# Performance work log

Measured on AMD Instinct MI355X. Metric: run time of the kernel, lower is better.

The kernel has to match this reference:

```python
import jax, jax.numpy as jnp
import numpy as np

N_NODES = 50000
N_EDGES = 1600000
IN_DIM = 128
HEADS = 8
OUT_C = 16  # per-head channels; HEADS*OUT_C == IN_DIM -> residual active
NEG_SLOPE = 0.2
BN_EPS = 1e-5


def setup_inputs() -> dict:
    key = jax.random.key(0)
    ks = jax.random.split(key, 8)
    x = jax.random.normal(ks[0], (N_NODES, IN_DIM), dtype=jnp.float32)
    edge_index = jax.random.randint(ks[1], (2, N_EDGES), 0, N_NODES, dtype=jnp.int64)
    # GATConv params (PyG: shared lin for src/dst on single-tensor input)
    W = jax.random.normal(ks[2], (IN_DIM, HEADS * OUT_C), dtype=jnp.float32) / np.sqrt(IN_DIM)
    att_src = jax.random.normal(ks[3], (HEADS, OUT_C), dtype=jnp.float32) / np.sqrt(OUT_C)
    att_dst = jax.random.normal(ks[4], (HEADS, OUT_C), dtype=jnp.float32) / np.sqrt(OUT_C)
    bias = jnp.zeros((HEADS * OUT_C,), dtype=jnp.float32)
    # BatchNorm1d affine params
    gamma = jnp.ones((HEADS * OUT_C,), dtype=jnp.float32)
    beta = jnp.zeros((HEADS * OUT_C,), dtype=jnp.float32)
    return {"x": x, "edge_index": edge_index, "W": W, "att_src": att_src,
            "att_dst": att_dst, "bias": bias, "gamma": gamma, "beta": beta}


def reference(x, edge_index, W, att_src, att_dst, bias, gamma, beta):
    N = x.shape[0]
    H, C = att_src.shape
    src, dst = edge_index[0], edge_index[1]

    xl = (x @ W).reshape(N, H, C)                      # [N,H,C]
    a_src = jnp.sum(xl * att_src[None], axis=-1)       # [N,H]
    a_dst = jnp.sum(xl * att_dst[None], axis=-1)       # [N,H]

    e = jax.nn.leaky_relu(a_src[src] + a_dst[dst], NEG_SLOPE)  # [E,H]
    # segment softmax over incoming edges of each dst node
    m = jax.ops.segment_max(e, dst, num_segments=N)    # [N,H], -inf for empty
    m = jnp.where(jnp.isfinite(m), m, 0.0)
    ex = jnp.exp(e - m[dst])                           # [E,H]
    denom = jax.ops.segment_sum(ex, dst, num_segments=N)
    alpha = ex / (denom[dst] + 1e-16)                  # [E,H]

    out = jax.ops.segment_sum(alpha[:, :, None] * xl[src], dst, num_segments=N)  # [N,H,C]
    h = out.reshape(N, H * C) + bias

    # BatchNorm1d (training mode: batch statistics, biased variance)
    mean = jnp.mean(h, axis=0)
    var = jnp.mean((h - mean) ** 2, axis=0)
    h = (h - mean) * jax.lax.rsqrt(var + BN_EPS) * gamma + beta

    h = jax.nn.relu(h)
    return x + h  # residual (in_dim == H*C)
```

## Files before the change

kernel.cpp:

```cpp
#include <hip/hip_runtime.h>
#include <hip/hip_fp16.h>
#include <math.h>

#define N_NODES 50000
#define N_EDGES 1600000
#define DIM 128
#define HEADS 8
#define NEG_SLOPE 0.2f
#define BN_EPS 1e-5f

typedef _Float16 f16x8 __attribute__((ext_vector_type(8)));
typedef float f32x4 __attribute__((ext_vector_type(4)));

__global__ void k_wprep(const float* __restrict__ W, __half* __restrict__ Wh,
                        int* __restrict__ bcur, float* __restrict__ gsums) {
    const int t = threadIdx.x;
    if (blockIdx.x == 0 && t < 256) bcur[t] = 0;
    if (blockIdx.x == 1 && t < 256) gsums[t] = 0.f;
    const int tid = blockIdx.x * 256 + t;
    const int g = tid >> 6;
    const int lane = tid & 63;
    const int nt = g >> 2, kt = g & 3;
    const int q = lane >> 4, n = lane & 15;
    #pragma unroll
    for (int j = 0; j < 8; ++j)
        Wh[(size_t)(g * 64 + lane) * 8 + j] =
            __float2half(W[(kt * 32 + q * 8 + j) * DIM + nt * 16 + n]);
}

__global__ __launch_bounds__(256) void k_lin(const float* __restrict__ x,
                      const __half* __restrict__ Wh, const float* __restrict__ att_s,
                      const float* __restrict__ att_d, __half* __restrict__ xlh,
                      float* __restrict__ a_src, float* __restrict__ a_dst) {
    const int wave = threadIdx.x >> 6;
    const int lane = threadIdx.x & 63;
    const int q = lane >> 4, n = lane & 15;
    const int nb = (blockIdx.x * 4 + wave) * 16;

    const int rowA = min(nb + n, N_NODES - 1);
    const float* xr = x + (size_t)rowA * DIM;
    f16x8 a[4];
    #pragma unroll
    for (int kt = 0; kt < 4; ++kt) {
        const float4 p0 = *(const float4*)(xr + kt * 32 + q * 8);
        const float4 p1 = *(const float4*)(xr + kt * 32 + q * 8 + 4);
        a[kt][0] = (_Float16)p0.x; a[kt][1] = (_Float16)p0.y;
        a[kt][2] = (_Float16)p0.z; a[kt][3] = (_Float16)p0.w;
        a[kt][4] = (_Float16)p1.x; a[kt][5] = (_Float16)p1.y;
        a[kt][6] = (_Float16)p1.z; a[kt][7] = (_Float16)p1.w;
    }

    f32x4 acc[8];
    #pragma unroll
    for (int nt = 0; nt < 8; ++nt) acc[nt] = (f32x4){0.f, 0.f, 0.f, 0.f};

    const f16x8* wb = (const f16x8*)Wh;
    #pragma unroll
    for (int nt = 0; nt < 8; ++nt) {
        #pragma unroll
        for (int kt = 0; kt < 4; ++kt) {
            const f16x8 b = wb[(nt * 4 + kt) * 64 + lane];
            acc[nt] = __builtin_amdgcn_mfma_f32_16x16x32_f16(a[kt], b, acc[nt], 0, 0, 0);
        }
    }

    const int r0 = nb + q * 4;
    #pragma unroll
    for (int nt = 0; nt < 8; ++nt) {
        const float as = att_s[nt * 16 + n];
        const float ad = att_d[nt * 16 + n];
        #pragma unroll
        for (int r = 0; r < 4; ++r) {
            const int row = r0 + r;
            const float v = acc[nt][r];
            float s = v * as;
            float d = v * ad;
            #pragma unroll
            for (int off = 8; off; off >>= 1) {
                s += __shfl_xor(s, off, 16);
                d += __shfl_xor(d, off, 16);
            }
            if (row < N_NODES) {
                xlh[(size_t)row * DIM + nt * 16 + n] = __float2half(v);
                if (n == 0) {
                    a_src[row * HEADS + nt] = s;
                    a_dst[row * HEADS + nt] = d;
                }
            }
        }
    }
}

#define NBUCK 196
#define SEGCAP 12288
#define CHUNK 8192
#define NB_A ((N_EDGES + CHUNK - 1) / CHUNK)

__global__ __launch_bounds__(1024) void k_binA(const int* __restrict__ ei,
                                               int* __restrict__ bcur,
                                               unsigned int* __restrict__ pairs) {
    __shared__ int hist[NBUCK], excl[NBUCK], gbase[NBUCK], cnt2[NBUCK];
    __shared__ int sc[256];
    __shared__ unsigned int buf[CHUNK];
    const int t = threadIdx.x;
    const int base = blockIdx.x * CHUNK;
    const int cnt = min(CHUNK, N_EDGES - base);

    for (int j = t; j < NBUCK; j += 1024) { hist[j] = 0; cnt2[j] = 0; }
    __syncthreads();
    for (int i = t * 4; i < cnt; i += 4096) {
        const int4 dv = *(const int4*)(ei + N_EDGES + base + i);
        atomicAdd(&hist[dv.x >> 8], 1);
        atomicAdd(&hist[dv.y >> 8], 1);
        atomicAdd(&hist[dv.z >> 8], 1);
        atomicAdd(&hist[dv.w >> 8], 1);
    }
    __syncthreads();
    if (t < 256) sc[t] = (t < NBUCK) ? hist[t] : 0;
    __syncthreads();
    for (int d = 1; d < 256; d <<= 1) {
        int xo = 0;
        if (t < 256 && t >= d) xo = sc[t - d];
        __syncthreads();
        if (t < 256) sc[t] += xo;
        __syncthreads();
    }
    if (t < NBUCK) {
        excl[t] = sc[t] - hist[t];
        gbase[t] = t * SEGCAP + atomicAdd(&bcur[t], hist[t]);
    }
    __syncthreads();
    for (int i = t * 4; i < cnt; i += 4096) {
        const int4 sv = *(const int4*)(ei + base + i);
        const int4 dv = *(const int4*)(ei + N_EDGES + base + i);
        const int ss[4] = {sv.x, sv.y, sv.z, sv.w};
        const int dd[4] = {dv.x, dv.y, dv.z, dv.w};
        #pragma unroll
        for (int k = 0; k < 4; ++k) {
            const int b = dd[k] >> 8;
            const int r = atomicAdd(&cnt2[b], 1);
            buf[excl[b] + r] = (unsigned int)ss[k] | ((unsigned int)(dd[k] & 255) << 16)
                             | ((unsigned int)b << 24);
        }
    }
    __syncthreads();
    for (int i = t; i < cnt; i += 1024) {
        const unsigned int u = buf[i];
        const int b = u >> 24;
        pairs[gbase[b] + (i - excl[b])] = u & 0xFFFFFF;
    }
}

__global__ __launch_bounds__(1024) void k_binB(const unsigned int* __restrict__ pairs,
                                               const int* __restrict__ bcur,
                                               unsigned short* __restrict__ csr,
                                               int2* __restrict__ nrange) {
    __shared__ int hist[256], eh[256], excl[256], cnt2[256];
    __shared__ int plen;
    __shared__ unsigned short out[SEGCAP];
    const int t = threadIdx.x;
    const int b = blockIdx.x;
    const int lo = b * SEGCAP;
    const int cnt = bcur[b];

    if (t < 256) { hist[t] = 0; cnt2[t] = 0; }
    __syncthreads();
    for (int i = t; i < cnt; i += 1024)
        atomicAdd(&hist[pairs[lo + i] >> 16], 1);
    __syncthreads();
    if (t < 256) { eh[t] = (hist[t] + 1) & ~1; excl[t] = eh[t]; }
    __syncthreads();
    for (int d = 1; d < 256; d <<= 1) {
        int xo = 0;
        if (t < 256 && t >= d) xo = excl[t - d];
        __syncthreads();
        if (t < 256) excl[t] += xo;
        __syncthreads();
    }
    if (t < 256) excl[t] -= eh[t];
    if (t == 255) plen = excl[255] + eh[255];
    __syncthreads();
    for (int i = t; i < cnt; i += 1024) {
        const unsigned int u = pairs[lo + i];
        const int dl = u >> 16;
        const int r = atomicAdd(&cnt2[dl], 1);
        out[excl[dl] + r] = (unsigned short)(u & 0xFFFF);
    }
    __syncthreads();
    const int pl = plen;
    for (int i = t; i < pl; i += 1024)
        csr[2 * lo + i] = out[i];
    if (t < 256) {
        const int node = (b << 8) + t;
        if (node < N_NODES) {
            int2 rg;
            rg.x = 2 * lo + excl[t];
            rg.y = rg.x + hist[t];
            nrange[node] = rg;
        }
    }
}

#define AGG_NPW 4
#define AGG_NB  (N_NODES / (4 * AGG_NPW))

__global__ __launch_bounds__(256) void k_aggr4(const int2* __restrict__ nrange,
                        const unsigned short* __restrict__ csr,
                        const float* __restrict__ a_src, const float* __restrict__ a_dst,
                        const __half* __restrict__ xlh, const float* __restrict__ bias,
                        float* __restrict__ y, float* __restrict__ gsums) {
    __shared__ float ch_s[DIM], ch_ss[DIM];
    const int t = threadIdx.x;
    const int wave = t >> 6, lane = t & 63;
    const int c2 = lane << 1;
    const int h = lane >> 3;
    if (t < DIM) { ch_s[t] = 0.f; ch_ss[t] = 0.f; }
    __syncthreads();

    const float b0 = bias[c2], b1 = bias[c2 + 1];
    float ps0 = 0.f, pss0 = 0.f, ps1 = 0.f, pss1 = 0.f;

    const int nb = (blockIdx.x * 4 + wave) * AGG_NPW;
    #pragma unroll
    for (int ii = 0; ii < AGG_NPW; ++ii) {
        const int d = nb + ii;
        const int2 rg = nrange[d];
        const int lo = rg.x, hi = rg.y;
        const float ad = a_dst[d * HEADS + h];
        float acc0 = 0.f, acc1 = 0.f, dsum = 0.f;
        int i = lo;
        for (; i + 8 <= hi; i += 8) {
            const int4 sp = *(const int4*)(csr + i);
            int s[8];
            s[0] = sp.x & 0xFFFF; s[1] = ((unsigned)sp.x) >> 16;
            s[2] = sp.y & 0xFFFF; s[3] = ((unsigned)sp.y) >> 16;
            s[4] = sp.z & 0xFFFF; s[5] = ((unsigned)sp.z) >> 16;
            s[6] = sp.w & 0xFFFF; s[7] = ((unsigned)sp.w) >> 16;
            float e[8];
            __half2 xv[8];
            #pragma unroll
            for (int j = 0; j < 8; ++j) e[j] = a_src[s[j] * HEADS + h] + ad;
            #pragma unroll
            for (int j = 0; j < 8; ++j)
                xv[j] = *(const __half2*)(xlh + (size_t)s[j] * DIM + c2);
            #pragma unroll
            for (int j = 0; j < 8; ++j) {
                const float w = __expf(fmaxf(e[j], NEG_SLOPE * e[j]));
                const float2 f = __half22float2(xv[j]);
                acc0 = fmaf(w, f.x, acc0);
                acc1 = fmaf(w, f.y, acc1);
                dsum += w;
            }
        }
        for (; i < hi; ++i) {
            const int s = csr[i];
            const float e = a_src[s * HEADS + h] + ad;
            const __half2 xv = *(const __half2*)(xlh + (size_t)s * DIM + c2);
            const float w = __expf(fmaxf(e, NEG_SLOPE * e));
            const float2 f = __half22float2(xv);
            acc0 = fmaf(w, f.x, acc0); acc1 = fmaf(w, f.y, acc1); dsum += w;
        }
        const float inv = 1.f / (dsum + 1e-16f);
        const float o0 = acc0 * inv, o1 = acc1 * inv;
        float2 o; o.x = o0; o.y = o1;
        *(float2*)(y + (size_t)d * DIM + c2) = o;
        const float h0 = o0 + b0, h1 = o1 + b1;
        ps0 += h0; pss0 += h0 * h0;
        ps1 += h1; pss1 += h1 * h1;
    }
    atomicAdd(&ch_s[c2], ps0);      atomicAdd(&ch_s[c2 + 1], ps1);
    atomicAdd(&ch_ss[c2], pss0);    atomicAdd(&ch_ss[c2 + 1], pss1);
    __syncthreads();
    atomicAdd(&gsums[t], (t < DIM) ? ch_s[t] : ch_ss[t - DIM]);
}

__global__ void k_final(float* __restrict__ y, const float* __restrict__ x,
                        const float* __restrict__ sums, const float* __restrict__ sumsq,
                        const float* __restrict__ gamma, const float* __restrict__ beta,
                        const float* __restrict__ bias) {
    const int q = blockIdx.x * blockDim.x + threadIdx.x;
    const int cq = q & (DIM / 4 - 1);
    const float4 sm = ((const float4*)sums)[cq];
    const float4 sq = ((const float4*)sumsq)[cq];
    const float4 gm = ((const float4*)gamma)[cq];
    const float4 bt = ((const float4*)beta)[cq];
    const float4 bs = ((const float4*)bias)[cq];
    float4 v = ((const float4*)y)[q];
    const float4 xv = ((const float4*)x)[q];
    const float inv_n = 1.f / (float)N_NODES;
#define BNC(c) { const float mean = sm.c * inv_n;                         \
                 const float var = sq.c * inv_n - mean * mean;            \
                 const float sc = rsqrtf(var + BN_EPS) * gm.c;            \
                 const float sh = bt.c + (bs.c - mean) * sc;              \
                 v.c = xv.c + fmaxf(v.c * sc + sh, 0.f); }
    BNC(x) BNC(y) BNC(z) BNC(w)
#undef BNC
    ((float4*)y)[q] = v;
}

extern "C" void kernel_launch(void* const* d_in, const int* in_sizes, int n_in,
                              void* d_out, int out_size, void* d_ws, size_t ws_size,
                              hipStream_t stream) {
    const float* x     = (const float*)d_in[0];
    const int*   ei    = (const int*)  d_in[1];
    const float* W     = (const float*)d_in[2];
    const float* att_s = (const float*)d_in[3];
    const float* att_d = (const float*)d_in[4];
    const float* bias  = (const float*)d_in[5];
    const float* gamma = (const float*)d_in[6];
    const float* beta  = (const float*)d_in[7];
    float* y = (float*)d_out;

    __half* xlh  = (__half*)d_ws;
    float* a_src = (float*)(xlh + (size_t)N_NODES * DIM);
    float* a_dst = a_src + (size_t)N_NODES * HEADS;
    float* sums  = a_dst + (size_t)N_NODES * HEADS;
    float* sumsq = sums  + DIM;
    int*   bcur  = (int*)(sumsq + DIM);
    int2*  nrange = (int2*)(bcur + 256);
    __half* Wh   = (__half*)(nrange + N_NODES);
    unsigned int* pairs = (unsigned int*)(Wh + 16384);
    unsigned short* csr = (unsigned short*)pairs;

    k_wprep<<<8, 256, 0, stream>>>(W, Wh, bcur, sums);
    k_lin<<<(N_NODES + 63) / 64, 256, 0, stream>>>(x, Wh, att_s, att_d, xlh, a_src, a_dst);
    k_binA<<<NB_A, 1024, 0, stream>>>(ei, bcur, pairs);
    k_binB<<<NBUCK, 1024, 0, stream>>>(pairs, bcur, csr, nrange);
    k_aggr4<<<AGG_NB, 256, 0, stream>>>(nrange, csr, a_src, a_dst, xlh, bias, y, sums);
    k_final<<<(size_t)N_NODES * DIM / 4 / 256, 256, 0, stream>>>(y, x, sums, sumsq,
                                                                 gamma, beta, bias);
}
```

Measured before the change: 258.4 us.

## Use one node per wave in aggregation and reduce BN stats via partials

The aggregation kernel now gives each wave a single destination node instead of four, so it launches four times as many blocks for more parallelism and latency hiding. Global atomics for the batch-norm sums are replaced by a per-block partials buffer plus a separate reduction kernel. CSR indices are loaded as individual shorts rather than packed int4 reads. The cost is an extra kernel launch, a partials buffer write and read, and more per-block setup and synchronisation overhead.

```diff
diff --git a/kernel.cpp b/kernel.cpp
--- a/kernel.cpp
+++ b/kernel.cpp
@@ -201,77 +201,76 @@
     }
 }
 
-#define AGG_NPW 4
-#define AGG_NB  (N_NODES / (4 * AGG_NPW))
-
-__global__ __launch_bounds__(256) void k_aggr4(const int2* __restrict__ nrange,
+#define AGG_NB (N_NODES / 4)
+
+__global__ __launch_bounds__(256) void k_aggr5(const int2* __restrict__ nrange,
                         const unsigned short* __restrict__ csr,
                         const float* __restrict__ a_src, const float* __restrict__ a_dst,
                         const __half* __restrict__ xlh, const float* __restrict__ bias,
-                        float* __restrict__ y, float* __restrict__ gsums) {
-    __shared__ float ch_s[DIM], ch_ss[DIM];
-    const int t = threadIdx.x;
-    const int wave = t >> 6, lane = t & 63;
+                        float* __restrict__ y, float* __restrict__ partials) {
+    __shared__ float ch[256];
+    const int t = threadIdx.x;
+    const int d = blockIdx.x * 4 + (t >> 6);
+    const int lane = t & 63;
     const int c2 = lane << 1;
     const int h = lane >> 3;
-    if (t < DIM) { ch_s[t] = 0.f; ch_ss[t] = 0.f; }
-    __syncthreads();
-
-    const float b0 = bias[c2], b1 = bias[c2 + 1];
-    float ps0 = 0.f, pss0 = 0.f, ps1 = 0.f, pss1 = 0.f;
-
-    const int nb = (blockIdx.x * 4 + wave) * AGG_NPW;
-    #pragma unroll
-    for (int ii = 0; ii < AGG_NPW; ++ii) {
-        const int d = nb + ii;
-        const int2 rg = nrange[d];
-        const int lo = rg.x, hi = rg.y;
-        const float ad = a_dst[d * HEADS + h];
-        float acc0 = 0.f, acc1 = 0.f, dsum = 0.f;
-        int i = lo;
-        for (; i + 8 <= hi; i += 8) {
-            const int4 sp = *(const int4*)(csr + i);
-            int s[8];
-            s[0] = sp.x & 0xFFFF; s[1] = ((unsigned)sp.x) >> 16;
-            s[2] = sp.y & 0xFFFF; s[3] = ((unsigned)sp.y) >> 16;
-            s[4] = sp.z & 0xFFFF; s[5] = ((unsigned)sp.z) >> 16;
-            s[6] = sp.w & 0xFFFF; s[7] = ((unsigned)sp.w) >> 16;
-            float e[8];
-            __half2 xv[8];
-            #pragma unroll
-            for (int j = 0; j < 8; ++j) e[j] = a_src[s[j] * HEADS + h] + ad;
-            #pragma unroll
-            for (int j = 0; j < 8; ++j)
-                xv[j] = *(const __half2*)(xlh + (size_t)s[j] * DIM + c2);
-            #pragma unroll
-            for (int j = 0; j < 8; ++j) {
-                const float w = __expf(fmaxf(e[j], NEG_SLOPE * e[j]));
-                const float2 f = __half22float2(xv[j]);
-                acc0 = fmaf(w, f.x, acc0);
-                acc1 = fmaf(w, f.y, acc1);
-                dsum += w;
-            }
-        }
-        for (; i < hi; ++i) {
-            const int s = csr[i];
-            const float e = a_src[s * HEADS + h] + ad;
-            const __half2 xv = *(const __half2*)(xlh + (size_t)s * DIM + c2);
-            const float w = __expf(fmaxf(e, NEG_SLOPE * e));
-            const float2 f = __half22float2(xv);
-            acc0 = fmaf(w, f.x, acc0); acc1 = fmaf(w, f.y, acc1); dsum += w;
-        }
-        const float inv = 1.f / (dsum + 1e-16f);
-        const float o0 = acc0 * inv, o1 = acc1 * inv;
-        float2 o; o.x = o0; o.y = o1;
-        *(float2*)(y + (size_t)d * DIM + c2) = o;
-        const float h0 = o0 + b0, h1 = o1 + b1;
-        ps0 += h0; pss0 += h0 * h0;
-        ps1 += h1; pss1 += h1 * h1;
-    }
-    atomicAdd(&ch_s[c2], ps0);      atomicAdd(&ch_s[c2 + 1], ps1);
-    atomicAdd(&ch_ss[c2], pss0);    atomicAdd(&ch_ss[c2 + 1], pss1);
-    __syncthreads();
-    atomicAdd(&gsums[t], (t < DIM) ? ch_s[t] : ch_ss[t - DIM]);
+    ch[t] = 0.f;
+    __syncthreads();
+
+    const int2 rg = nrange[d];
+    const int lo = rg.x, hi = rg.y;
+    const float ad = a_dst[d * HEADS + h];
+    float acc0 = 0.f, acc1 = 0.f, dsum = 0.f;
+    int i = lo;
+    for (; i + 8 <= hi; i += 8) {
+        int s[8];
+        float e[8];
+        __half2 xv[8];
+        #pragma unroll
+        for (int j = 0; j < 8; ++j) s[j] = csr[i + j];
+        #pragma unroll
+        for (int j = 0; j < 8; ++j) e[j] = a_src[s[j] * HEADS + h] + ad;
+        #pragma unroll
+        for (int j = 0; j < 8; ++j)
+            xv[j] = *(const __half2*)(xlh + (size_t)s[j] * DIM + c2);
+        #pragma unroll
+        for (int j = 0; j < 8; ++j) {
+            const float w = __expf(fmaxf(e[j], NEG_SLOPE * e[j]));
+            const float2 f = __half22float2(xv[j]);
+            acc0 = fmaf(w, f.x, acc0);
+            acc1 = fmaf(w, f.y, acc1);
+            dsum += w;
+        }
+    }
+    for (; i < hi; ++i) {
+        const int s = csr[i];
+        const float e = a_src[s * HEADS + h] + ad;
+        const __half2 xv = *(const __half2*)(xlh + (size_t)s * DIM + c2);
+        const float w = __expf(fmaxf(e, NEG_SLOPE * e));
+        const float2 f = __half22float2(xv);
+        acc0 = fmaf(w, f.x, acc0); acc1 = fmaf(w, f.y, acc1); dsum += w;
+    }
+    const float inv = 1.f / (dsum + 1e-16f);
+    const float o0 = acc0 * inv, o1 = acc1 * inv;
+    float2 o; o.x = o0; o.y = o1;
+    *(float2*)(y + (size_t)d * DIM + c2) = o;
+
+    const float h0 = o0 + bias[c2], h1 = o1 + bias[c2 + 1];
+    atomicAdd(&ch[c2], h0);
+    atomicAdd(&ch[c2 + 1], h1);
+    atomicAdd(&ch[DIM + c2], h0 * h0);
+    atomicAdd(&ch[DIM + c2 + 1], h1 * h1);
+    __syncthreads();
+    partials[(size_t)blockIdx.x * 256 + t] = ch[t];
+}
+
+#define NRED 100
+__global__ void k_red(const float* __restrict__ partials, float* __restrict__ gsums) {
+    const int t = threadIdx.x;
+    float v = 0.f;
+    for (int r = blockIdx.x; r < AGG_NB; r += NRED)
+        v += partials[(size_t)r * 256 + t];
+    atomicAdd(&gsums[t], v);
 }
 
 __global__ void k_final(float* __restrict__ y, const float* __restrict__ x,
@@ -321,12 +320,14 @@
     __half* Wh   = (__half*)(nrange + N_NODES);
     unsigned int* pairs = (unsigned int*)(Wh + 16384);
     unsigned short* csr = (unsigned short*)pairs;
+    float* partials = (float*)(pairs + (size_t)NBUCK * SEGCAP);
 
     k_wprep<<<8, 256, 0, stream>>>(W, Wh, bcur, sums);
     k_lin<<<(N_NODES + 63) / 64, 256, 0, stream>>>(x, Wh, att_s, att_d, xlh, a_src, a_dst);
     k_binA<<<NB_A, 1024, 0, stream>>>(ei, bcur, pairs);
     k_binB<<<NBUCK, 1024, 0, stream>>>(pairs, bcur, csr, nrange);
-    k_aggr4<<<AGG_NB, 256, 0, stream>>>(nrange, csr, a_src, a_dst, xlh, bias, y, sums);
+    k_aggr5<<<AGG_NB, 256, 0, stream>>>(nrange, csr, a_src, a_dst, xlh, bias, y, partials);
+    k_red<<<NRED, 256, 0, stream>>>(partials, sums);
     k_final<<<(size_t)N_NODES * DIM / 4 / 256, 256, 0, stream>>>(y, x, sums, sumsq,
                                                                  gamma, beta, bias);
 }
```

Result: slower. 291.1 us (+12.7%).
